# Optimization experiments

Measured on AMD Instinct MI355X. Metric: run time of the kernel, lower is better.

## Reference

```python
import jax, jax.numpy as jnp
import numpy as np

LATENT, ACTION, HIDDEN, TEMB = 256, 32, 1024, 128
BATCH, NTRAJ, HORIZON = 1024, 16, 5
EPI_W, PRAG_W, CONS_W, GAMMA = 1.0, 1.0, 0.1, 0.99
LOG2PI = float(np.log(2.0 * np.pi))


def _dense_init(key, fan_in, fan_out):
    return jax.random.normal(key, (fan_in, fan_out), dtype=jnp.float32) / np.sqrt(fan_in)


def time_embed(t):
    # sinusoidal embedding, TEMB dims, like ValueNetwork(time_embed_dim=128)
    half = TEMB // 2
    freqs = jnp.exp(-np.log(10000.0) * jnp.arange(half, dtype=jnp.float32) / half)
    ang = t[:, None] * freqs[None, :]  # [B, half]
    return jnp.concatenate([jnp.sin(ang), jnp.cos(ang)], axis=-1)  # [B, TEMB]


def setup_inputs() -> dict:
    key = jax.random.key(0)
    ks = jax.random.split(key, 12)
    return {
        "latent": jax.random.normal(ks[0], (BATCH, LATENT), dtype=jnp.float32),
        "noise": jax.random.normal(ks[1], (NTRAJ, HORIZON, BATCH, ACTION), dtype=jnp.float32),
        # DiffusionConditionedPolicy (state-dependent std): trunk + mean/log_std heads
        "pW1": _dense_init(ks[2], LATENT, HIDDEN), "pb1": jnp.zeros((HIDDEN,), jnp.float32),
        "pW2": _dense_init(ks[3], HIDDEN, HIDDEN), "pb2": jnp.zeros((HIDDEN,), jnp.float32),
        "pWm": _dense_init(ks[4], HIDDEN, ACTION), "pbm": jnp.zeros((ACTION,), jnp.float32),
        "pWs": _dense_init(ks[5], HIDDEN, ACTION), "pbs": jnp.zeros((ACTION,), jnp.float32),
        # LatentDynamicsModel: 3-layer MLP on [latent, action] -> delta
        "dW1": _dense_init(ks[6], LATENT + ACTION, HIDDEN), "db1": jnp.zeros((HIDDEN,), jnp.float32),
        "dW2": _dense_init(ks[7], HIDDEN, HIDDEN), "db2": jnp.zeros((HIDDEN,), jnp.float32),
        "dW3": _dense_init(ks[8], HIDDEN, LATENT), "db3": jnp.zeros((LATENT,), jnp.float32),
        # ValueNetwork: 3-layer MLP on [latent, time_embed] -> scalar
        "vW1": _dense_init(ks[9], LATENT + TEMB, HIDDEN), "vb1": jnp.zeros((HIDDEN,), jnp.float32),
        "vW2": _dense_init(ks[10], HIDDEN, HIDDEN), "vb2": jnp.zeros((HIDDEN,), jnp.float32),
        "vW3": _dense_init(ks[11], HIDDEN, 1), "vb3": jnp.zeros((1,), jnp.float32),
    }


def _efe_forward(latent, noise, pW1, pb1, pW2, pb2, pWm, pbm, pWs, pbs,
                 dW1, db1, dW2, db2, dW3, db3, vW1, vb1, vW2, vb2, vW3, vb3):
    def policy(z, eps):
        h = jax.nn.silu(z @ pW1 + pb1)
        h = jax.nn.silu(h @ pW2 + pb2)
        mean = h @ pWm + pbm
        log_std = jnp.clip(h @ pWs + pbs, -5.0, 2.0)
        action = mean + jnp.exp(log_std) * eps  # reparameterized sample
        # Normal entropy per-dim, summed over action dim
        ent = jnp.sum(0.5 * (1.0 + LOG2PI) + log_std, axis=-1)
        return action, ent

    def dynamics(z, a):
        h = jnp.concatenate([z, a], axis=-1)
        h = jax.nn.silu(h @ dW1 + db1)
        h = jax.nn.silu(h @ dW2 + db2)
        return h @ dW3 + db3  # delta latent

    def value(z, tvec):
        h = jnp.concatenate([z, time_embed(tvec)], axis=-1)
        h = jax.nn.silu(h @ vW1 + vb1)
        h = jax.nn.silu(h @ vW2 + vb2)
        return (h @ vW3 + vb3)[..., 0]  # squeeze(-1)

    def step(z, inp):
        eps_t, t = inp
        action, ent = policy(z, eps_t)
        z_next = z + dynamics(z, action)  # predict_next_latent
        # _compute_latent_kl on normalized latents
        zn = z / (jnp.linalg.norm(z, axis=-1, keepdims=True) + 1e-8)
        pn = z_next / (jnp.linalg.norm(z_next, axis=-1, keepdims=True) + 1e-8)
        kl = 0.5 * jnp.sum((zn - pn) ** 2, axis=-1)
        epistemic = jnp.log1p(kl)
        tvec = jnp.full((z.shape[0],), 0.0, dtype=z.dtype) + t
        pragmatic = value(z_next, tvec)
        consistency = -ent
        step_efe = EPI_W * epistemic + PRAG_W * pragmatic + CONS_W * consistency
        return z_next, step_efe

    ts = jnp.arange(HORIZON, dtype=jnp.float32)

    def rollout(eps_traj):  # eps_traj: [H, B, A]
        _, efes = jax.lax.scan(step, latent, (eps_traj, ts))  # efes: [H, B]
        disc = GAMMA ** ts  # discount_factor ** t
        return jnp.sum(disc[:, None] * efes, axis=0)  # traj_efe: [B]

    traj_efe = jax.vmap(rollout)(noise)  # [NTRAJ, B]
    total_efe = jnp.mean(traj_efe, axis=0)  # sum of traj_efe / num_trajectories
    return total_efe


def reference(latent, noise, pW1, pb1, pW2, pb2, pWm, pbm, pWs, pbs,
              dW1, db1, dW2, db2, dW3, db3, vW1, vb1, vW2, vb2, vW3, vb3):
    return _efe_forward(latent, noise, pW1, pb1, pW2, pb2, pWm, pbm, pWs, pbs,
                        dW1, db1, dW2, db2, dW3, db3, vW1, vb1, vW2, vb2, vW3, vb3)
```

## Files before the change

### kernel.cpp

```cpp
#include <hip/hip_runtime.h>
#include <cstdint>
#include <cstddef>
#include <cmath>


typedef __bf16 bf16;
typedef __attribute__((ext_vector_type(8))) __bf16 bf16x8;
typedef __attribute__((ext_vector_type(4))) __bf16 bf16x4;
typedef __attribute__((ext_vector_type(4))) float f32x4;

static constexpr int BATCH = 1024, NTRAJ = 16, HORIZON = 5;
static constexpr int MR = NTRAJ * BATCH;
static constexpr float ENT_C = 1.4189385332046727f;
static constexpr float SUMDISC = 4.90099501f;

__device__ __forceinline__ void gld_lds16(const bf16* g, const bf16* l) {
  typedef __attribute__((address_space(1))) const uint32_t gq_t;
  typedef __attribute__((address_space(3))) uint32_t lq_t;
  gq_t* gp = (gq_t*)(uintptr_t)g;
  lq_t* lp = (lq_t*)(uint32_t)(uintptr_t)l;
  __builtin_amdgcn_global_load_lds(gp, lp, 16, 0, 0);
}

__device__ __forceinline__ float silu(float x) {
  return x * __builtin_amdgcn_rcpf(1.f + __expf(-x));
}

#define MFMA16(a, b, c) __builtin_amdgcn_mfma_f32_16x16x32_bf16((a), (b), (c), 0, 0, 0)
#define SBAR() __builtin_amdgcn_s_barrier()
#define SCHED0() __builtin_amdgcn_sched_barrier(0)
#define VMCNT(n) asm volatile("s_waitcnt vmcnt(" #n ")" ::: "memory")
#define LGKMCNT0() asm volatile("s_waitcnt lgkmcnt(0)" ::: "memory")

__global__ __launch_bounds__(256) void gemm128(
    const bf16* __restrict__ A, int lda, int K, const bf16* __restrict__ Bt,
    const float* __restrict__ bias, int act_cols,
    bf16* __restrict__ C1, bf16* __restrict__ C2, int ldc) {
  __shared__ alignas(16) bf16 PA[2][2][128 * 32];
  __shared__ alignas(16) bf16 PB[2][2][128 * 32];
  const int tid = threadIdx.x, wave = tid >> 6, lane = tid & 63;
  const int quad = lane >> 4, l16 = lane & 15;
  const int rowBlk = blockIdx.x * 128, colBlk = blockIdx.y * 128;
  const int wr = wave >> 1, wc = wave & 1;
  const int srow = lane >> 2;
  const int skel = (((lane & 3) ^ ((lane >> 3) & 3)) * 8);
  const int qsw = quad ^ ((l16 >> 1) & 3);

  const bf16* gA0 = A + (size_t)(rowBlk + wave * 32 + srow) * lda + skel;
  const bf16* gA1 = gA0 + (size_t)16 * lda;
  const bf16* gB0 = Bt + (size_t)(colBlk + wave * 32 + srow) * K + skel;
  const bf16* gB1 = gB0 + (size_t)16 * K;

#define STG128(t, b)                                      \
  do {                                                    \
    const int k0_ = (t)*64;                               \
    gld_lds16(gA0 + k0_, &PA[b][0][wave * 1024]);         \
    gld_lds16(gA1 + k0_, &PA[b][0][wave * 1024 + 512]);   \
    gld_lds16(gA0 + k0_ + 32, &PA[b][1][wave * 1024]);    \
    gld_lds16(gA1 + k0_ + 32, &PA[b][1][wave * 1024 + 512]); \
    gld_lds16(gB0 + k0_, &PB[b][0][wave * 1024]);         \
    gld_lds16(gB1 + k0_, &PB[b][0][wave * 1024 + 512]);   \
    gld_lds16(gB0 + k0_ + 32, &PB[b][1][wave * 1024]);    \
    gld_lds16(gB1 + k0_ + 32, &PB[b][1][wave * 1024 + 512]); \
  } while (0)

  f32x4 acc[4][4] = {};
  const int nt = K >> 6;
  STG128(0, 0);
  STG128(1, 1);
  VMCNT(8);
  SBAR();
  SCHED0();
  for (int t = 0; t < nt; ++t) {
    const int b = t & 1;
#pragma unroll
    for (int ks = 0; ks < 2; ++ks) {
      const bf16* aRd = &PA[b][ks][(wr * 64 + l16) * 32 + qsw * 8];
      const bf16* bRd = &PB[b][ks][(wc * 64 + l16) * 32 + qsw * 8];
      bf16x8 af[4], bfr[4];
#pragma unroll
      for (int i = 0; i < 4; ++i) {
        af[i] = *(const bf16x8*)(aRd + i * 16 * 32);
        bfr[i] = *(const bf16x8*)(bRd + i * 16 * 32);
      }
#pragma unroll
      for (int mi = 0; mi < 4; ++mi)
#pragma unroll
        for (int ni = 0; ni < 4; ++ni)
          acc[mi][ni] = MFMA16(bfr[ni], af[mi], acc[mi][ni]);
    }
    if (t == nt - 1) break;
    SBAR();
    SCHED0();
    if (t + 2 < nt) {
      STG128(t + 2, b);
      VMCNT(8);
    } else {
      VMCNT(0);
    }
    SBAR();
    SCHED0();
  }
#undef STG128

  const bool doAct = (colBlk < act_cols);
  bf16* const Cp = doAct ? C1 : C2;
  const int cShift = doAct ? 0 : act_cols;
#pragma unroll
  for (int mi = 0; mi < 4; ++mi) {
    const int row = rowBlk + wr * 64 + mi * 16 + l16;
#pragma unroll
    for (int ni = 0; ni < 4; ++ni) {
      const int col0 = colBlk + wc * 64 + ni * 16 + quad * 4;
      const f32x4 bb = *(const f32x4*)(bias + col0);
      bf16x4 o;
#pragma unroll
      for (int r = 0; r < 4; ++r) {
        float x = acc[mi][ni][r] + bb[r];
        if (doAct) x = silu(x);
        o[r] = (bf16)x;
      }
      *(bf16x4*)(Cp + (size_t)row * ldc + (col0 - cShift)) = o;
    }
  }
}

__global__ __launch_bounds__(256) void gemm_pd1v(
    const bf16* __restrict__ A, const bf16* __restrict__ Bt,
    const float* __restrict__ pdb1, const float* __restrict__ vbiasT,
    bf16* __restrict__ Ha, bf16* __restrict__ Hp, bf16* __restrict__ Hv) {
  __shared__ alignas(16) bf16 As0[128 * 32], As1[128 * 32];
  __shared__ alignas(16) bf16 Bs0[128 * 32], Bs1[128 * 32];
  const int tid = threadIdx.x, wave = tid >> 6, lane = tid & 63;
  const int quad = lane >> 4, l16 = lane & 15;
  const int rowBlk = blockIdx.x * 128, colBlk = blockIdx.y * 128;
  const int wr = wave >> 1, wc = wave & 1;
  const int srow = lane >> 2;
  const int skel = (((lane & 3) ^ ((lane >> 3) & 3)) * 8);
  const int qsw = quad ^ ((l16 >> 1) & 3);

  const bf16* gA0 = A + (size_t)(rowBlk + wave * 32 + srow) * 256 + skel;
  const bf16* gA1 = gA0 + (size_t)16 * 256;
  const bf16* gB0 = Bt + (size_t)(colBlk + wave * 32 + srow) * 256 + skel;
  const bf16* gB1 = gB0 + (size_t)16 * 256;
  bf16* const lA0 = As0 + wave * 32 * 32;
  bf16* const lA0b = As0 + (wave * 32 + 16) * 32;
  bf16* const lA1 = As1 + wave * 32 * 32;
  bf16* const lA1b = As1 + (wave * 32 + 16) * 32;
  bf16* const lB0 = Bs0 + wave * 32 * 32;
  bf16* const lB0b = Bs0 + (wave * 32 + 16) * 32;
  bf16* const lB1 = Bs1 + wave * 32 * 32;
  bf16* const lB1b = Bs1 + (wave * 32 + 16) * 32;

  f32x4 acc[4][4] = {};
  for (int k0 = 0; k0 < 256; k0 += 64) {
    gld_lds16(gA0 + k0, lA0);
    gld_lds16(gA1 + k0, lA0b);
    gld_lds16(gA0 + k0 + 32, lA1);
    gld_lds16(gA1 + k0 + 32, lA1b);
    gld_lds16(gB0 + k0, lB0);
    gld_lds16(gB1 + k0, lB0b);
    gld_lds16(gB0 + k0 + 32, lB1);
    gld_lds16(gB1 + k0 + 32, lB1b);
    __syncthreads();
#pragma unroll
    for (int ks = 0; ks < 2; ++ks) {
      const bf16* aRd = (ks ? As1 : As0) + (wr * 64 + l16) * 32 + qsw * 8;
      const bf16* bRd = (ks ? Bs1 : Bs0) + (wc * 64 + l16) * 32 + qsw * 8;
      bf16x8 af[4], bfr[4];
#pragma unroll
      for (int i = 0; i < 4; ++i) {
        af[i] = *(const bf16x8*)(aRd + i * 16 * 32);
        bfr[i] = *(const bf16x8*)(bRd + i * 16 * 32);
      }
#pragma unroll
      for (int mi = 0; mi < 4; ++mi)
#pragma unroll
        for (int ni = 0; ni < 4; ++ni)
          acc[mi][ni] = MFMA16(bfr[ni], af[mi], acc[mi][ni]);
    }
    __syncthreads();
  }

  const int seg = colBlk >> 10;
  bf16* const Cp = (seg == 0) ? Ha : (seg == 1) ? Hp : Hv;
  const int cShift = seg << 10;
  const float* const bp = (seg == 2) ? (vbiasT - 2048) : pdb1;
#pragma unroll
  for (int mi = 0; mi < 4; ++mi) {
    const int row = rowBlk + wr * 64 + mi * 16 + l16;
#pragma unroll
    for (int ni = 0; ni < 4; ++ni) {
      const int col0 = colBlk + wc * 64 + ni * 16 + quad * 4;
      const f32x4 bb = *(const f32x4*)(bp + col0);
      bf16x4 o;
#pragma unroll
      for (int r = 0; r < 4; ++r) {
        float x = acc[mi][ni][r] + bb[r];
        if (seg != 1) x = silu(x);
        o[r] = (bf16)x;
      }
      *(bf16x4*)(Cp + (size_t)row * 1024 + (col0 - cShift)) = o;
    }
  }
}

template <int NT, int EPI>
__device__ __forceinline__ void gemm256_body(
    const bf16* __restrict__ A, const bf16* __restrict__ Bt, int rowBlk,
    int colBlk, const float* __restrict__ bias, const float* __restrict__ aux,
    bf16* __restrict__ C1, float* __restrict__ efe, float disc,
    bf16 (*sAB)[2][256 * 64]) {
  constexpr int K = NT * 64;
  const int tid = threadIdx.x, wave = tid >> 6, lane = tid & 63;
  const int quad = lane >> 4, l16 = lane & 15;
  const int wr = wave >> 2, wc = wave & 3;

  const int j8 = lane >> 3;
  const int c16e = ((lane & 7) ^ j8) * 8;
  const bf16* gAs = A + (size_t)(rowBlk + wave * 16 + j8) * K + c16e;
  const bf16* gBs = Bt + (size_t)(colBlk + wave * 16 + j8) * K + c16e;

#define STAGE_A(hh, tt, bb)                                           \
  do {                                                                \
    const bf16* g_ = gAs + (hh) * 128 * K + (tt) * 64;                \
    bf16* l_ = &sAB[(bb)][0][((hh) * 128 + wave * 16) * 64];          \
    gld_lds16(g_, l_);                                                \
    gld_lds16(g_ + 8 * K, l_ + 8 * 64);                               \
  } while (0)
#define STAGE_B(hh, tt, bb)                                           \
  do {                                                                \
    const bf16* g_ = gBs + (hh) * 128 * K + (tt) * 64;                \
    bf16* l_ = &sAB[(bb)][1][((hh) * 128 + wave * 16) * 64];          \
    gld_lds16(g_, l_);                                                \
    gld_lds16(g_ + 8 * K, l_ + 8 * 64);                               \
  } while (0)

  const int k0x = (quad * 8) ^ ((l16 & 7) << 3);
  const int aOff = (wr * 128 + l16) * 64 + k0x;
  const int bOff = (wc * 64 + l16) * 64 + k0x;

  bf16x8 bAf[4][2], bBf[2][2], bB2f[2][2];
  f32x4 acc[8][4] = {};

  STAGE_A(0, 0, 0);
  STAGE_A(1, 0, 0);
  STAGE_B(0, 0, 0);
  STAGE_B(1, 0, 0);
  STAGE_B(0, 1, 1);
  STAGE_B(1, 1, 1);
  VMCNT(4);
  SBAR();
  SCHED0();

#pragma unroll 2
  for (int t = 0; t < NT; ++t) {
    const int buf = t & 1;
    const bf16* lA = &sAB[buf][0][0];
    const bf16* lB = &sAB[buf][1][0];

#pragma unroll
    for (int m = 0; m < 4; ++m)
#pragma unroll
      for (int ks = 0; ks < 2; ++ks)
        bAf[m][ks] = *(const bf16x8*)(lA + ((aOff + m * 1024) ^ (ks << 5)));
#pragma unroll
    for (int n = 0; n < 2; ++n)
#pragma unroll
      for (int ks = 0; ks < 2; ++ks)
        bBf[n][ks] = *(const bf16x8*)(lB + ((bOff + n * 1024) ^ (ks << 5)));
    if (t + 1 < NT) STAGE_A(0, t + 1, buf ^ 1);
    SBAR();
    LGKMCNT0();
    SCHED0();
    __builtin_amdgcn_s_setprio(1);
#pragma unroll
    for (int ks = 0; ks < 2; ++ks)
#pragma unroll
      for (int m = 0; m < 4; ++m)
#pragma unroll
        for (int n = 0; n < 2; ++n)
          acc[m][n] = MFMA16(bBf[n][ks], bAf[m][ks], acc[m][n]);
    __builtin_amdgcn_s_setprio(0);
    SBAR();
    SCHED0();

#pragma unroll
    for (int n = 0; n < 2; ++n)
#pragma unroll
      for (int ks = 0; ks < 2; ++ks)
        bB2f[n][ks] =
            *(const bf16x8*)(lB + ((bOff + (n + 2) * 1024) ^ (ks << 5)));
    if (t + 1 < NT) STAGE_A(1, t + 1, buf ^ 1);
    SBAR();
    LGKMCNT0();
    SCHED0();
    __builtin_amdgcn_s_setprio(1);
#pragma unroll
    for (int ks = 0; ks < 2; ++ks)
#pragma unroll
      for (int m = 0; m < 4; ++m)
#pragma unroll
        for (int n = 0; n < 2; ++n)
          acc[m][n + 2] = MFMA16(bB2f[n][ks], bAf[m][ks], acc[m][n + 2]);
    __builtin_amdgcn_s_setprio(0);
    SBAR();
    SCHED0();

#pragma unroll
    for (int m = 0; m < 4; ++m)
#pragma unroll
      for (int ks = 0; ks < 2; ++ks)
        bAf[m][ks] =
            *(const bf16x8*)(lA + ((aOff + (m + 4) * 1024) ^ (ks << 5)));
    if (t + 2 < NT) STAGE_B(0, t + 2, buf);
    SBAR();
    LGKMCNT0();
    SCHED0();
    __builtin_amdgcn_s_setprio(1);
#pragma unroll
    for (int ks = 0; ks < 2; ++ks)
#pragma unroll
      for (int m = 0; m < 4; ++m)
#pragma unroll
        for (int n = 0; n < 2; ++n)
          acc[m + 4][n + 2] =
              MFMA16(bB2f[n][ks], bAf[m][ks], acc[m + 4][n + 2]);
    __builtin_amdgcn_s_setprio(0);
    SBAR();
    SCHED0();

    if (t + 2 < NT) STAGE_B(1, t + 2, buf);
    SBAR();
    SCHED0();
    __builtin_amdgcn_s_setprio(1);
#pragma unroll
    for (int ks = 0; ks < 2; ++ks)
#pragma unroll
      for (int m = 0; m < 4; ++m)
#pragma unroll
        for (int n = 0; n < 2; ++n)
          acc[m + 4][n] = MFMA16(bBf[n][ks], bAf[m][ks], acc[m + 4][n]);
    __builtin_amdgcn_s_setprio(0);
    if (t < NT - 2) {
      VMCNT(4);
    } else {
      VMCNT(0);
    }
    SBAR();
    SCHED0();
  }
#undef STAGE_A
#undef STAGE_B

  if constexpr (EPI == 0) {
#pragma unroll
    for (int m = 0; m < 8; ++m) {
      const int row = rowBlk + wr * 128 + m * 16 + l16;
#pragma unroll
      for (int n = 0; n < 4; ++n) {
        const int gcol = colBlk + wc * 64 + n * 16 + quad * 4;
        const f32x4 bb = *(const f32x4*)(bias + gcol);
        bf16x4 o;
#pragma unroll
        for (int r = 0; r < 4; ++r) o[r] = (bf16)silu(acc[m][n][r] + bb[r]);
        *(bf16x4*)(C1 + (size_t)row * 1024 + gcol) = o;
      }
    }
  } else {
#pragma unroll
    for (int m = 0; m < 8; ++m) {
      const int row = rowBlk + wr * 128 + m * 16 + l16;
      float p = 0.f;
#pragma unroll
      for (int n = 0; n < 4; ++n) {
        const int gcol = colBlk + wc * 64 + n * 16 + quad * 4;
        const f32x4 bb = *(const f32x4*)(bias + gcol);
        const f32x4 w3 = *(const f32x4*)(aux + gcol);
#pragma unroll
        for (int r = 0; r < 4; ++r) p += silu(acc[m][n][r] + bb[r]) * w3[r];
      }
      p += __shfl_xor(p, 16);
      p += __shfl_xor(p, 32);
      if (quad == 0) atomicAdd(efe + row, disc * p);
    }
  }
}

template <int NT, int EPI>
__global__ __launch_bounds__(512, 2) void gemm256(
    const bf16* __restrict__ A, const bf16* __restrict__ Bt, int nCol,
    const float* __restrict__ bias, const float* __restrict__ aux,
    bf16* __restrict__ C1, float* __restrict__ efe, float disc) {
  static_assert(NT >= 2, "need at least 2 K-tiles");
  __shared__ alignas(16) bf16 sAB[2][2][256 * 64];
  const int nwg = gridDim.x, flat = blockIdx.x;
  const int lid = (flat & 7) * (nwg >> 3) + (flat >> 3);
  const int rowBlk = (lid / nCol) * 256, colBlk = (lid % nCol) * 256;
  gemm256_body<NT, EPI>(A, Bt, rowBlk, colBlk, bias, aux, C1, efe, disc, sAB);
}

template <int NT>
__global__ __launch_bounds__(512, 2) void gemm256_dual(
    const bf16* __restrict__ A0, const bf16* __restrict__ Bt0,
    const float* __restrict__ bias0, bf16* __restrict__ C0,
    const bf16* __restrict__ A1, const bf16* __restrict__ Bt1,
    const float* __restrict__ bias1, const float* __restrict__ aux1,
    float* __restrict__ efe, float disc) {
  __shared__ alignas(16) bf16 sAB[2][2][256 * 64];
  const int flat = blockIdx.x;
  const int seq = (flat & 7) * 32 + (flat >> 3);
  const int rowBlk = (seq >> 2) * 256, colBlk = (seq & 3) * 256;
  gemm256_body<NT, 0>(A0, Bt0, rowBlk, colBlk, bias0, nullptr, C0, nullptr,
                      0.f, sAB);
  gemm256_body<NT, 1>(A1, Bt1, rowBlk, colBlk, bias1, aux1, nullptr, efe,
                      disc, sAB);
}

__global__ __launch_bounds__(256) void gemm_dyn3(
    const bf16* __restrict__ A, const bf16* __restrict__ Bt,
    const float* __restrict__ db3, float* __restrict__ Zf,
    bf16* __restrict__ Zb, float* __restrict__ s_n, float* __restrict__ s_c) {
  __shared__ alignas(16) bf16 PA[2][2][64 * 32];
  __shared__ alignas(16) bf16 PB[2][2][128 * 32];
  const int tid = threadIdx.x, wave = tid >> 6, lane = tid & 63;
  const int quad = lane >> 4, l16 = lane & 15;
  const int rowBlk = blockIdx.x * 64, colBlk = blockIdx.y * 128;
  const int srow = lane >> 2;
  const int skel = (((lane & 3) ^ ((lane >> 3) & 3)) * 8);
  const int qsw = quad ^ ((l16 >> 1) & 3);

  const bf16* gA = A + (size_t)(rowBlk + wave * 16 + srow) * 1024 + skel;
  const bf16* gB0 = Bt + (size_t)(colBlk + wave * 32 + srow) * 1024 + skel;
  const bf16* gB1 = gB0 + (size_t)16 * 1024;

#define STGD(t, b)                                        \
  do {                                                    \
    const int k0_ = (t)*64;                               \
    gld_lds16(gA + k0_, &PA[b][0][wave * 512]);           \
    gld_lds16(gA + k0_ + 32, &PA[b][1][wave * 512]);      \
    gld_lds16(gB0 + k0_, &PB[b][0][wave * 1024]);         \
    gld_lds16(gB1 + k0_, &PB[b][0][wave * 1024 + 512]);   \
    gld_lds16(gB0 + k0_ + 32, &PB[b][1][wave * 1024]);    \
    gld_lds16(gB1 + k0_ + 32, &PB[b][1][wave * 1024 + 512]); \
  } while (0)

  f32x4 acc[8] = {};
  STGD(0, 0);
  STGD(1, 1);
  VMCNT(6);
  SBAR();
  SCHED0();
#pragma unroll 2
  for (int t = 0; t < 16; ++t) {
    const int b = t & 1;
#pragma unroll
    for (int ks = 0; ks < 2; ++ks) {
      const bf16* aRd = &PA[b][ks][(wave * 16 + l16) * 32 + qsw * 8];
      const bf16* bRd = &PB[b][ks][l16 * 32 + qsw * 8];
      const bf16x8 af = *(const bf16x8*)aRd;
#pragma unroll
      for (int ni = 0; ni < 8; ++ni) {
        const bf16x8 bfr = *(const bf16x8*)(bRd + ni * 16 * 32);
        acc[ni] = MFMA16(bfr, af, acc[ni]);
      }
    }
    if (t == 15) break;
    SBAR();
    SCHED0();
    if (t < 14) {
      STGD(t + 2, b);
      VMCNT(6);
    } else {
      VMCNT(0);
    }
    SBAR();
    SCHED0();
  }
#undef STGD

  const int row = rowBlk + wave * 16 + l16;
  float pn = 0.f, pc = 0.f;
#pragma unroll
  for (int ni = 0; ni < 8; ++ni) {
    const int col0 = colBlk + ni * 16 + quad * 4;
    const f32x4 b4 = *(const f32x4*)(db3 + col0);
    float* zp = Zf + (size_t)row * 256 + col0;
    const f32x4 z = *(const f32x4*)zp;
    f32x4 zn;
    bf16x4 o;
#pragma unroll
    for (int r = 0; r < 4; ++r) {
      zn[r] = z[r] + acc[ni][r] + b4[r];
      pn += zn[r] * zn[r];
      pc += z[r] * zn[r];
      o[r] = (bf16)zn[r];
    }
    *(f32x4*)zp = zn;
    *(bf16x4*)(Zb + (size_t)row * 256 + col0) = o;
  }
  pn += __shfl_xor(pn, 16);
  pn += __shfl_xor(pn, 32);
  pc += __shfl_xor(pc, 16);
  pc += __shfl_xor(pc, 32);
  if (quad == 0) {
    atomicAdd(s_n + row, pn);
    atomicAdd(s_c + row, pc);
  }
}

__global__ void kl_batch(const float* __restrict__ sz0,
                         const float* __restrict__ snAll,
                         const float* __restrict__ scAll,
                         float* __restrict__ efe) {
  const int m = blockIdx.x * 256 + threadIdx.x;
  float sz = sz0[m];
  float disc = 1.f, acc = 0.f;
  for (int t = 0; t < HORIZON; ++t) {
    const float sn = snAll[t * MR + m], sc = scAll[t * MR + m];
    const float nz = sqrtf(sz) + 1e-8f, nn = sqrtf(sn) + 1e-8f;
    const float kl =
        0.5f * (sz / (nz * nz) + sn / (nn * nn) - 2.f * sc / (nz * nn));
    acc += disc * log1pf(fmaxf(kl, 0.f));
    sz = sn;
    disc *= 0.99f;
  }
  efe[m] += acc;
}

__global__ __launch_bounds__(256) void heads4(
    const bf16* __restrict__ H, const bf16* __restrict__ Wt,
    const float* __restrict__ pbm, const float* __restrict__ pbs,
    const float* __restrict__ noise, const bf16* __restrict__ preD,
    const bf16* __restrict__ dW1at, bf16* __restrict__ Hd,
    float* __restrict__ efe, int t, float disc, int rmask) {
  __shared__ alignas(16) bf16 As[2][4 * 16 * 32];
  __shared__ alignas(16) bf16 Bs[2][4 * 64 * 32];
  __shared__ alignas(16) bf16 LAct[16 * 32];
  const int tid = threadIdx.x, wave = tid >> 6, lane = tid & 63;
  const int quad = lane >> 4, l16 = lane & 15;
  const int rowBlk = blockIdx.x * 16;
  const int srow = lane >> 2;
  const int skel = (((lane & 3) ^ ((lane >> 3) & 3)) * 8);
  const int qsw = quad ^ ((l16 >> 1) & 3);
  const int kw = wave * 256;

  const bf16* gA = H + (size_t)((rowBlk + srow) & rmask) * 1024 + kw + skel;

#define STGH(kt, b)                                                         \
  do {                                                                      \
    gld_lds16(gA + (kt) * 32, &As[b][wave * 512]);                          \
    _Pragma("unroll") for (int j = 0; j < 4; ++j) gld_lds16(                \
        Wt + (size_t)(j * 16 + srow) * 1024 + kw + (kt) * 32 + skel,        \
        &Bs[b][wave * 2048 + j * 512]);                                     \
  } while (0)

  f32x4 acc[4] = {};
  STGH(0, 0);
  STGH(1, 1);
#pragma unroll
  for (int kt = 0; kt < 8; ++kt) {
    const int b = kt & 1;
    if (kt < 7) {
      VMCNT(5);
    } else {
      VMCNT(0);
    }
    SCHED0();
    const bf16x8 af =
        *(const bf16x8*)(&As[b][wave * 512] + l16 * 32 + qsw * 8);
#pragma unroll
    for (int ni = 0; ni < 4; ++ni) {
      const bf16x8 bfr =
          *(const bf16x8*)(&Bs[b][wave * 2048] + (ni * 16 + l16) * 32 + qsw * 8);
      acc[ni] = MFMA16(bfr, af, acc[ni]);
    }
    SCHED0();
    if (kt < 6) {
      LGKMCNT0();
      STGH(kt + 2, b);
    }
  }
#undef STGH

  float* red = (float*)Bs;
#pragma unroll
  for (int ni = 0; ni < 4; ++ni)
    *(f32x4*)(red + wave * 1024 + ni * 256 + lane * 4) = acc[ni];
  __syncthreads();
#pragma unroll
  for (int ni = 0; ni < 4; ++ni) {
    f32x4 s = *(const f32x4*)(red + ni * 256 + lane * 4);
#pragma unroll
    for (int w2 = 1; w2 < 4; ++w2) {
      const f32x4 p = *(const f32x4*)(red + w2 * 1024 + ni * 256 + lane * 4);
#pragma unroll
      for (int r = 0; r < 4; ++r) s[r] += p[r];
    }
    acc[ni] = s;
  }

  const int row = rowBlk + l16;
  const int n = row >> 10, b2 = row & 1023;
  float ent = 0.f;
#pragma unroll
  for (int ni = 0; ni < 2; ++ni) {
    const int col0 = ni * 16 + quad * 4;
    const f32x4 bm4 = *(const f32x4*)(pbm + col0);
    const f32x4 bs4 = *(const f32x4*)(pbs + col0);
    const f32x4 ep4 =
        *(const f32x4*)(noise + (((size_t)(n * 5 + t) * 1024 + b2) * 32 + col0));
    bf16x4 o;
#pragma unroll
    for (int r = 0; r < 4; ++r) {
      const float mean = acc[ni][r] + bm4[r];
      float ls = acc[ni + 2][r] + bs4[r];
      ls = fminf(fmaxf(ls, -5.f), 2.f);
      o[r] = (bf16)(mean + __expf(ls) * ep4[r]);
      ent += ENT_C + ls;
    }
    if (wave == 0) *(bf16x4*)(LAct + l16 * 32 + col0) = o;
  }
  ent += __shfl_xor(ent, 16);
  ent += __shfl_xor(ent, 32);
  if (wave == 0 && quad == 0) efe[row] += disc * (-0.1f) * ent;
  __syncthreads();

  const int prow = row & rmask;
  const bf16x8 af2 = *(const bf16x8*)(LAct + l16 * 32 + quad * 8);
#pragma unroll 4
  for (int ci = 0; ci < 16; ++ci) {
    const int ct = wave * 16 + ci;
    const bf16x8 wf =
        *(const bf16x8*)(dW1at + (size_t)(ct * 16 + l16) * 32 + quad * 8);
    f32x4 a = {};
    a = MFMA16(wf, af2, a);
    const int col0 = ct * 16 + quad * 4;
    const bf16x4 pd = *(const bf16x4*)(preD + (size_t)prow * 1024 + col0);
    bf16x4 o;
#pragma unroll
    for (int r = 0; r < 4; ++r) o[r] = (bf16)silu(a[r] + (float)pd[r]);
    *(bf16x4*)(Hd + (size_t)row * 1024 + col0) = o;
  }
}

__global__ __launch_bounds__(256) void prep_tr(
    const float* __restrict__ pW1, const float* __restrict__ dW1,
    const float* __restrict__ vW1, const float* __restrict__ pW2,
    const float* __restrict__ dW2, const float* __restrict__ dW3,
    const float* __restrict__ vW2, const float* __restrict__ pWm,
    const float* __restrict__ pWs, const float* __restrict__ pb1,
    const float* __restrict__ db1, const float* __restrict__ vb1,
    const float* __restrict__ latent, bf16* __restrict__ pdW1vt,
    bf16* __restrict__ pW2t, bf16* __restrict__ pHt,
    bf16* __restrict__ dW1at, bf16* __restrict__ dW2t,
    bf16* __restrict__ dW3t, bf16* __restrict__ vW2t,
    float* __restrict__ pdb1, float* __restrict__ vbias,
    float* __restrict__ Zf, bf16* __restrict__ Zb0, float* __restrict__ efe,
    float* __restrict__ sz0, float* __restrict__ snAll,
    float* __restrict__ scAll) {
  int bid = blockIdx.x;
  if (bid == 1072) {
    for (int i = threadIdx.x; i < 2048; i += 256)
      pdb1[i] = (i < 1024) ? pb1[i] : db1[i - 1024];
    return;
  }
  if (bid >= 1073 && bid < 1093) {
    const int idx = (bid - 1073) * 256 + threadIdx.x;
    const int t = idx >> 10, j = idx & 1023;
    float s = vb1[j];
    const float lt = (float)t;
    for (int i = 0; i < 64; ++i) {
      const float f = expf(-9.210340371976184f * (float)i / 64.f);
      const float ang = lt * f;
      s += sinf(ang) * vW1[(size_t)(256 + i) * 1024 + j];
      s += cosf(ang) * vW1[(size_t)(256 + 64 + i) * 1024 + j];
    }
    vbias[idx] = s;
    return;
  }
  if (bid >= 1093) {
    const int wave = threadIdx.x >> 6, lane = threadIdx.x & 63;
    const int row = (bid - 1093) * 4 + wave;
    const f32x4 z = *(const f32x4*)(latent + (size_t)(row & 1023) * 256 + lane * 4);
    *(f32x4*)(Zf + (size_t)row * 256 + lane * 4) = z;
    if (row < 1024) {
      bf16x4 o = {(bf16)z[0], (bf16)z[1], (bf16)z[2], (bf16)z[3]};
      *(bf16x4*)(Zb0 + (size_t)row * 256 + lane * 4) = o;
    }
    float s = z[0] * z[0] + z[1] * z[1] + z[2] * z[2] + z[3] * z[3];
#pragma unroll
    for (int m = 1; m < 64; m <<= 1) s += __shfl_xor(s, m);
    if (lane == 0) {
      sz0[row] = s;
      efe[row] = 0.f;
    }
    if (lane < HORIZON) {
      snAll[lane * MR + row] = 0.f;
      scAll[lane * MR + row] = 0.f;
    }
    return;
  }
  const float* in;
  bf16* out;
  int K, N, ldin, ro = 0;
  if (bid < 64) { in = pW1; out = pdW1vt; K = 256; N = 1024; ldin = 1024; }
  else if (bid < 128) { bid -= 64; in = dW1; out = pdW1vt + 1024 * 256; K = 256; N = 1024; ldin = 1024; }
  else if (bid < 192) { bid -= 128; in = vW1; out = pdW1vt + 2048 * 256; K = 256; N = 1024; ldin = 1024; }
  else if (bid < 448) { bid -= 192; in = pW2; out = pW2t; K = 1024; N = 1024; ldin = 1024; }
  else if (bid < 704) { bid -= 448; in = dW2; out = dW2t; K = 1024; N = 1024; ldin = 1024; }
  else if (bid < 960) { bid -= 704; in = vW2; out = vW2t; K = 1024; N = 1024; ldin = 1024; }
  else if (bid < 1024) { bid -= 960; in = dW3; out = dW3t; K = 1024; N = 256; ldin = 256; }
  else if (bid < 1040) { bid -= 1024; in = dW1; out = dW1at; K = 32; N = 1024; ldin = 1024; ro = 256; }
  else if (bid < 1056) { bid -= 1040; in = pWm; out = pHt; K = 1024; N = 32; ldin = 32; }
  else { bid -= 1056; in = pWs; out = pHt + 32 * 1024; K = 1024; N = 32; ldin = 32; }

  const int ktiles = (K + 63) >> 6;
  const int k0 = (bid % ktiles) * 64, n0 = (bid / ktiles) * 64;
  __shared__ float tile[64][65];
  const int tx = threadIdx.x & 63, ty = threadIdx.x >> 6;
#pragma unroll
  for (int i = 0; i < 16; ++i) {
    const int k = k0 + ty + i * 4;
    if (k < K && n0 + tx < N)
      tile[ty + i * 4][tx] = in[(size_t)(ro + k) * ldin + n0 + tx];
  }
  __syncthreads();
#pragma unroll
  for (int i = 0; i < 16; ++i) {
    const int n = n0 + ty + i * 4;
    if (n < N && k0 + tx < K)
      out[(size_t)n * K + k0 + tx] = (bf16)tile[tx][ty + i * 4];
  }
}

__global__ void finalize(const float* __restrict__ efe,
                         const float* __restrict__ vb3,
                         float* __restrict__ out) {
  const int b = blockIdx.x * 256 + threadIdx.x;
  float s = 0.f;
#pragma unroll
  for (int n = 0; n < 16; ++n) s += efe[n * 1024 + b];
  out[b] = s * (1.f / 16.f) + SUMDISC * vb3[0];
}

extern "C" void kernel_launch(void* const* d_in, const int* in_sizes, int n_in,
                              void* d_out, int out_size, void* d_ws,
                              size_t ws_size, hipStream_t stream) {
  const float* latent = (const float*)d_in[0];
  const float* noise = (const float*)d_in[1];
  const float* pW1 = (const float*)d_in[2];
  const float* pb1 = (const float*)d_in[3];
  const float* pW2 = (const float*)d_in[4];
  const float* pb2 = (const float*)d_in[5];
  const float* pWm = (const float*)d_in[6];
  const float* pbm = (const float*)d_in[7];
  const float* pWs = (const float*)d_in[8];
  const float* pbs = (const float*)d_in[9];
  const float* dW1 = (const float*)d_in[10];
  const float* db1 = (const float*)d_in[11];
  const float* dW2 = (const float*)d_in[12];
  const float* db2 = (const float*)d_in[13];
  const float* dW3 = (const float*)d_in[14];
  const float* db3 = (const float*)d_in[15];
  const float* vW1 = (const float*)d_in[16];
  const float* vb1 = (const float*)d_in[17];
  const float* vW2 = (const float*)d_in[18];
  const float* vb2 = (const float*)d_in[19];
  const float* vW3 = (const float*)d_in[20];
  const float* vb3 = (const float*)d_in[21];

  char* w = (char*)d_ws;
  size_t off = 0;
  auto take = [&](size_t bytes) -> void* {
    void* p = (void*)(w + off);
    off = (off + bytes + 255) & ~(size_t)255;
    return p;
  };
  bf16* pdW1vt = (bf16*)take(3072ull * 256 * 2);
  float* pdb1 = (float*)take(2048ull * 4);
  bf16* pW2t = (bf16*)take(1024ull * 1024 * 2);
  bf16* pHt = (bf16*)take(64ull * 1024 * 2);
  bf16* dW1at = (bf16*)take(1024ull * 32 * 2);
  bf16* dW2t = (bf16*)take(1024ull * 1024 * 2);
  bf16* dW3t = (bf16*)take(256ull * 1024 * 2);
  bf16* vW2t = (bf16*)take(1024ull * 1024 * 2);
  float* vbias = (float*)take(5ull * 1024 * 4);
  bf16* Zb0 = (bf16*)take(1024ull * 256 * 2);
  bf16* Zb = (bf16*)take((size_t)MR * 256 * 2);
  float* Zf = (float*)take((size_t)MR * 256 * 4);
  float* efe = (float*)take((size_t)MR * 4);
  float* sz0 = (float*)take((size_t)MR * 4);
  float* snAll = (float*)take(5ull * MR * 4);
  float* scAll = (float*)take(5ull * MR * 4);
  bf16* Ha = (bf16*)take((size_t)MR * 1024 * 2);
  bf16* Hc = (bf16*)take((size_t)MR * 1024 * 2);
  bf16* Hp = (bf16*)take((size_t)MR * 1024 * 2);
  bf16* Hv = (bf16*)take((size_t)MR * 1024 * 2);
  bf16* vW1t = pdW1vt + (size_t)2048 * 256;

  const dim3 blk(256), blk2(512);
  const int BIG = 1 << 30;
  prep_tr<<<dim3(1093 + MR / 4), blk, 0, stream>>>(
      pW1, dW1, vW1, pW2, dW2, dW3, vW2, pWm, pWs, pb1, db1, vb1, latent,
      pdW1vt, pW2t, pHt, dW1at, dW2t, dW3t, vW2t, pdb1, vbias, Zf, Zb0, efe,
      sz0, snAll, scAll);

  float disc = 1.f, dprev = 1.f;
  for (int s = 0; s < HORIZON; ++s) {
    const int rmask = (s == 0) ? 1023 : 0x7FFFFFFF;
    if (s == 0) {
      gemm128<<<dim3(8, 16), blk, 0, stream>>>(Zb0, 256, 256, pdW1vt, pdb1,
                                               1024, Ha, Hp, 1024);
      gemm128<<<dim3(8, 8), blk, 0, stream>>>(Ha, 1024, 1024, pW2t, pb2, BIG,
                                              Hc, Hc, 1024);
    } else {
      gemm_pd1v<<<dim3(128, 24), blk, 0, stream>>>(
          Zb, pdW1vt, pdb1, vbias + (s - 1) * 1024, Ha, Hp, Hv);
      gemm256_dual<16><<<dim3(256), blk2, 0, stream>>>(
          Ha, pW2t, pb2, Hc, Hv, vW2t, vb2, vW3, efe, dprev);
    }
    heads4<<<dim3(MR / 16), blk, 0, stream>>>(Hc, pHt, pbm, pbs, noise, Hp,
                                              dW1at, Ha, efe, s, disc, rmask);
    gemm256<16, 0><<<dim3(256), blk2, 0, stream>>>(Ha, dW2t, 4, db2, nullptr,
                                                   Hc, nullptr, 0.f);
    gemm_dyn3<<<dim3(MR / 64, 2), blk, 0, stream>>>(
        Hc, dW3t, db3, Zf, Zb, snAll + (size_t)s * MR, scAll + (size_t)s * MR);
    dprev = disc;
    disc *= 0.99f;
  }

  kl_batch<<<dim3(MR / 256), blk, 0, stream>>>(sz0, snAll, scAll, efe);

  gemm128<<<dim3(128, 8), blk, 0, stream>>>(Zb, 256, 256, vW1t,
                                            vbias + 4 * 1024, BIG, Hv, Hv,
                                            1024);
  gemm256<16, 1><<<dim3(256), blk2, 0, stream>>>(Hv, vW2t, 4, vb2, vW3,
                                                 nullptr, efe, dprev);
  finalize<<<dim3(4), blk, 0, stream>>>(efe, vb3, (float*)d_out);
}
```

Before: 1.021 ms.

## Make first-layer fused GEMM persistent with resident weight slice and triple-buffered A

Replaces the 128x128-tiled grid GEMM for the fused policy/dynamics/value first layer with a persistent 256-block kernel. Each block loads a 192-column slice of the weight matrix (full K=256) into LDS once, then streams 32-row A chunks through a three-deep buffer, using XCD-aware block-to-work mapping. This aims to remove repeated weight reloads and per-tile launch overhead, and to overlap A loads with MFMA work. In exchange, each chunk produces only a small 32x192 output tile per iteration with two barriers, so MFMA density per sync is low.

```diff
diff --git a/kernel.cpp b/kernel.cpp
--- a/kernel.cpp
+++ b/kernel.cpp
@@ -125,84 +125,94 @@
   }
 }
 
-__global__ __launch_bounds__(256) void gemm_pd1v(
+__global__ __launch_bounds__(512) void gemm_pd1v_ps(
     const bf16* __restrict__ A, const bf16* __restrict__ Bt,
     const float* __restrict__ pdb1, const float* __restrict__ vbiasT,
     bf16* __restrict__ Ha, bf16* __restrict__ Hp, bf16* __restrict__ Hv) {
-  __shared__ alignas(16) bf16 As0[128 * 32], As1[128 * 32];
-  __shared__ alignas(16) bf16 Bs0[128 * 32], Bs1[128 * 32];
+  __shared__ alignas(16) bf16 Bs[8 * 192 * 32];
+  __shared__ alignas(16) bf16 As[3][8 * 32 * 32];
   const int tid = threadIdx.x, wave = tid >> 6, lane = tid & 63;
   const int quad = lane >> 4, l16 = lane & 15;
-  const int rowBlk = blockIdx.x * 128, colBlk = blockIdx.y * 128;
-  const int wr = wave >> 1, wc = wave & 1;
+  const int wr = wave >> 2, wc = wave & 3;
   const int srow = lane >> 2;
   const int skel = (((lane & 3) ^ ((lane >> 3) & 3)) * 8);
   const int qsw = quad ^ ((l16 >> 1) & 3);
 
-  const bf16* gA0 = A + (size_t)(rowBlk + wave * 32 + srow) * 256 + skel;
-  const bf16* gA1 = gA0 + (size_t)16 * 256;
-  const bf16* gB0 = Bt + (size_t)(colBlk + wave * 32 + srow) * 256 + skel;
-  const bf16* gB1 = gB0 + (size_t)16 * 256;
-  bf16* const lA0 = As0 + wave * 32 * 32;
-  bf16* const lA0b = As0 + (wave * 32 + 16) * 32;
-  bf16* const lA1 = As1 + wave * 32 * 32;
-  bf16* const lA1b = As1 + (wave * 32 + 16) * 32;
-  bf16* const lB0 = Bs0 + wave * 32 * 32;
-  bf16* const lB0b = Bs0 + (wave * 32 + 16) * 32;
-  bf16* const lB1 = Bs1 + wave * 32 * 32;
-  bf16* const lB1b = Bs1 + (wave * 32 + 16) * 32;
-
-  f32x4 acc[4][4] = {};
-  for (int k0 = 0; k0 < 256; k0 += 64) {
-    gld_lds16(gA0 + k0, lA0);
-    gld_lds16(gA1 + k0, lA0b);
-    gld_lds16(gA0 + k0 + 32, lA1);
-    gld_lds16(gA1 + k0 + 32, lA1b);
-    gld_lds16(gB0 + k0, lB0);
-    gld_lds16(gB1 + k0, lB0b);
-    gld_lds16(gB0 + k0 + 32, lB1);
-    gld_lds16(gB1 + k0 + 32, lB1b);
-    __syncthreads();
-#pragma unroll
-    for (int ks = 0; ks < 2; ++ks) {
-      const bf16* aRd = (ks ? As1 : As0) + (wr * 64 + l16) * 32 + qsw * 8;
-      const bf16* bRd = (ks ? Bs1 : Bs0) + (wc * 64 + l16) * 32 + qsw * 8;
-      bf16x8 af[4], bfr[4];
-#pragma unroll
-      for (int i = 0; i < 4; ++i) {
-        af[i] = *(const bf16x8*)(aRd + i * 16 * 32);
-        bfr[i] = *(const bf16x8*)(bRd + i * 16 * 32);
+  const int flat = blockIdx.x;
+  const int xcd = flat & 7, idx = flat >> 3;
+  const int rg = xcd * 2 + (idx & 1);
+  const int cp = idx >> 1;
+  const int colBase = cp * 192;
+  const int row0 = rg * 1024;
+
+#pragma unroll
+  for (int i = 0; i < 12; ++i)
+    gld_lds16(Bt + (size_t)(colBase + i * 16 + srow) * 256 + wave * 32 + skel,
+              Bs + (wave * 192 + i * 16) * 32);
+
+#define STG_A(c, bb)                                                        \
+  do {                                                                      \
+    const bf16* g_ =                                                        \
+        A + (size_t)(row0 + (c) * 32 + srow) * 256 + wave * 32 + skel;      \
+    bf16* l_ = As[bb] + (wave * 32) * 32;                                   \
+    gld_lds16(g_, l_);                                                      \
+    gld_lds16(g_ + 16 * 256, l_ + 16 * 32);                                 \
+  } while (0)
+
+  STG_A(0, 0);
+  STG_A(1, 1);
+  STG_A(2, 2);
+  VMCNT(4);
+  SBAR();
+  SCHED0();
+
+  int b = 0;
+  for (int c = 0; c < 32; ++c) {
+    f32x4 acc[3] = {};
+    const bf16* lA = As[b];
+#pragma unroll
+    for (int kg = 0; kg < 8; ++kg) {
+      const bf16x8 af =
+          *(const bf16x8*)(lA + (kg * 32 + wr * 16 + l16) * 32 + qsw * 8);
+#pragma unroll
+      for (int n = 0; n < 3; ++n) {
+        const bf16x8 bfr = *(const bf16x8*)(
+            Bs + (kg * 192 + wc * 48 + n * 16 + l16) * 32 + qsw * 8);
+        acc[n] = MFMA16(bfr, af, acc[n]);
       }
-#pragma unroll
-      for (int mi = 0; mi < 4; ++mi)
-#pragma unroll
-        for (int ni = 0; ni < 4; ++ni)
-          acc[mi][ni] = MFMA16(bfr[ni], af[mi], acc[mi][ni]);
-    }
-    __syncthreads();
-  }
-
-  const int seg = colBlk >> 10;
-  bf16* const Cp = (seg == 0) ? Ha : (seg == 1) ? Hp : Hv;
-  const int cShift = seg << 10;
-  const float* const bp = (seg == 2) ? (vbiasT - 2048) : pdb1;
-#pragma unroll
-  for (int mi = 0; mi < 4; ++mi) {
-    const int row = rowBlk + wr * 64 + mi * 16 + l16;
-#pragma unroll
-    for (int ni = 0; ni < 4; ++ni) {
-      const int col0 = colBlk + wc * 64 + ni * 16 + quad * 4;
-      const f32x4 bb = *(const f32x4*)(bp + col0);
+    }
+    SBAR();
+    SCHED0();
+    if (c + 3 < 32) {
+      STG_A(c + 3, b);
+      VMCNT(4);
+    } else if (c + 2 < 32) {
+      VMCNT(2);
+    } else if (c + 1 < 32) {
+      VMCNT(0);
+    }
+    SBAR();
+    SCHED0();
+    const int row = row0 + c * 32 + wr * 16 + l16;
+#pragma unroll
+    for (int n = 0; n < 3; ++n) {
+      const int gcol = colBase + wc * 48 + n * 16 + quad * 4;
+      const int seg = gcol >> 10;
+      bf16* const Cp = (seg == 0) ? Ha : (seg == 1) ? Hp : Hv;
+      const float* const bp = (seg == 2) ? (vbiasT - 2048) : pdb1;
+      const f32x4 bb = *(const f32x4*)(bp + gcol);
       bf16x4 o;
 #pragma unroll
       for (int r = 0; r < 4; ++r) {
-        float x = acc[mi][ni][r] + bb[r];
+        float x = acc[n][r] + bb[r];
         if (seg != 1) x = silu(x);
         o[r] = (bf16)x;
       }
-      *(bf16x4*)(Cp + (size_t)row * 1024 + (col0 - cShift)) = o;
-    }
-  }
+      *(bf16x4*)(Cp + (size_t)row * 1024 + (gcol - (seg << 10))) = o;
+    }
+    b = (b == 2) ? 0 : b + 1;
+  }
+#undef STG_A
 }
 
 template <int NT, int EPI>
@@ -815,7 +825,7 @@
       gemm128<<<dim3(8, 8), blk, 0, stream>>>(Ha, 1024, 1024, pW2t, pb2, BIG,
                                               Hc, Hc, 1024);
     } else {
-      gemm_pd1v<<<dim3(128, 24), blk, 0, stream>>>(
+      gemm_pd1v_ps<<<dim3(256), blk2, 0, stream>>>(
           Zb, pdW1vt, pdb1, vbias + (s - 1) * 1024, Ha, Hp, Hv);
       gemm256_dual<16><<<dim3(256), blk2, 0, stream>>>(
           Ha, pW2t, pb2, Hc, Hv, vW2t, vb2, vW3, efe, dprev);
```

After: 1.041 ms. About the same (+2.0%).
